# Performance work log

Measured on AMD Instinct MI355X. Metric: run time of the kernel, lower is better.

The kernel has to match this reference:

```python
import jax, jax.numpy as jnp
import numpy as np

FIELDS, NUM, CAT = 39, 13, 26
D, M, V, B, DEEP = 16, 16, 100000, 4096, 400
LEFT, RIGHT = np.triu_indices(FIELDS, k=1)  # pair indices, Q = 741
Q = LEFT.size
EPS = 1e-5


def setup_inputs() -> dict:
    key = jax.random.key(0)
    ks = jax.random.split(key, 18)
    xi = jax.random.randint(ks[0], (B, CAT), 0, V)
    xv = jax.random.uniform(ks[1], (B, NUM), dtype=jnp.float32)
    # 2nd-order embedding tables, stacked since all fields share vocab size
    emb_tables = jax.random.normal(ks[2], (FIELDS, V, D), dtype=jnp.float32) * 0.1
    T3 = jax.random.normal(ks[3], (D, M, D), dtype=jnp.float32) * 0.05
    T2 = jax.random.normal(ks[4], (M, D * D), dtype=jnp.float32) * 0.05
    gc = jax.random.normal(ks[5], (Q,), dtype=jnp.float32)
    fi_w = jax.random.normal(ks[6], (Q * M, DEEP), dtype=jnp.float32) * 0.01
    fi_b = jnp.zeros((DEEP,), dtype=jnp.float32)
    fi_gamma = jnp.ones((DEEP,), dtype=jnp.float32)
    fi_beta = jnp.zeros((DEEP,), dtype=jnp.float32)
    emb_w = jax.random.normal(ks[7], (FIELDS * D, DEEP), dtype=jnp.float32) * 0.02
    emb_b = jnp.zeros((DEEP,), dtype=jnp.float32)
    emb_gamma = jnp.ones((DEEP,), dtype=jnp.float32)
    emb_beta = jnp.zeros((DEEP,), dtype=jnp.float32)
    fc_w = jax.random.normal(ks[8], (2 * DEEP, 1), dtype=jnp.float32) * 0.05
    fc_b = jnp.zeros((1,), dtype=jnp.float32)
    return {"xi": xi, "xv": xv, "emb_tables": emb_tables, "T3": T3, "T2": T2,
            "gc": gc, "fi_w": fi_w, "fi_b": fi_b, "fi_gamma": fi_gamma, "fi_beta": fi_beta,
            "emb_w": emb_w, "emb_b": emb_b, "emb_gamma": emb_gamma, "emb_beta": emb_beta,
            "fc_w": fc_w, "fc_b": fc_b}


def _bn(x, gamma, beta):
    # BatchNorm1d in training mode: batch statistics, biased variance
    mean = jnp.mean(x, axis=0)
    var = jnp.var(x, axis=0)
    return gamma * (x - mean) * jax.lax.rsqrt(var + EPS) + beta


def reference(xi, xv, emb_tables, T3, T2, gc, fi_w, fi_b, fi_gamma, fi_beta,
              emb_w, emb_b, emb_gamma, emb_beta, fc_w, fc_b):
    # numerical fields: embedding row 0 scaled by the raw value
    num_part = xv[:, :, None] * emb_tables[:NUM, 0, :][None]          # [B, 13, D]
    # categorical fields: per-field gather
    cat_part = emb_tables[NUM + jnp.arange(CAT)[None, :], xi]          # [B, 26, D]
    fm2 = jnp.concatenate([num_part, cat_part], axis=1)               # [B, 39, D]
    vi = fm2[:, LEFT]                                                  # [B, Q, D]
    vj = fm2[:, RIGHT]                                                 # [B, Q, D]
    # einsum('bqd,dmd,bqd->bm'): repeated d on T3 takes its diagonal -> [D, M]
    T3diag = jnp.einsum('dmd->dm', T3)
    ga = jnp.einsum('bqd,bqd,dm->bm', vi, vj, T3diag)                  # [B, M]
    ga = jax.nn.softmax(ga, axis=1)
    # T1 = einsum('bm,mn->bmn'); s = einsum('bqd,bmn,bqd->bqm') sums T1 over n
    t1_rowsum = ga * jnp.sum(T2, axis=1)[None, :]                      # [B, M]
    pair_dot = jnp.einsum('bqd,bqd->bq', vi, vj)                       # [B, Q]
    s = pair_dot[:, :, None] * t1_rowsum[:, None, :]                   # [B, Q, M]
    sh = (s * gc[None, :, None]).reshape(-1, Q * M)                    # [B, Q*M]
    th = jax.nn.relu(_bn(sh @ fi_w + fi_b, fi_gamma, fi_beta))         # [B, DEEP]
    emb = fm2.reshape(-1, FIELDS * D)                                  # [B, 39*D]
    emb = jax.nn.relu(_bn(emb @ emb_w + emb_b, emb_gamma, emb_beta))   # [B, DEEP]
    out = jnp.concatenate([th, emb], axis=1) @ fc_w + fc_b             # [B, 1]
    return jnp.sum(jax.nn.sigmoid(out), axis=1)                        # [B]
```

## Files before the change

kernel.cpp:

```cpp
#include <hip/hip_runtime.h>
#include <hip/hip_bf16.h>

#define BATCH 4096
#define FIELDS_ 39
#define NUMF 13
#define CATF 26
#define DD 16
#define MM 16
#define VV 100000
#define DEEP_ 400
#define QQ 741
#define QPAD 768
#define KE 624
#define KEP 640
#define NEP 512
#define N1 6400
#define NKTE 20
#define NT_ 24
#define EPS_ 1e-5f

#define OFF_ABF 0
#define OFF_T   (BATCH*QPAD/2)
#define OFF_W2  (OFF_T + BATCH*MM)
#define OFF_WE  (OFF_W2 + N1*QPAD/2)
#define OFF_FMB (OFF_WE + NEP*KEP/2)
#define OFF_TH  (OFF_FMB + BATCH*KEP/2)
#define OFF_EMB (OFF_TH + BATCH*DEEP_)
#define OFF_ACC (OFF_EMB + BATCH*DEEP_)

typedef __attribute__((ext_vector_type(8))) short bf16x8;
typedef __attribute__((ext_vector_type(4))) float f32x4;

__device__ __forceinline__ ushort f2bf(float v) {
    union { float f; unsigned u; } x; x.f = v;
    unsigned r = x.u + 0x7fff + ((x.u >> 16) & 1);
    return (ushort)(r >> 16);
}
__device__ __forceinline__ unsigned pack2(float a, float b) {
    return (unsigned)f2bf(a) | ((unsigned)f2bf(b) << 16);
}
__device__ __forceinline__ void async16(void* lds, const void* g) {
    __builtin_amdgcn_global_load_lds(
        (const __attribute__((address_space(1))) unsigned int*)g,
        (__attribute__((address_space(3))) unsigned int*)lds,
        16, 0, 0);
}

__global__ __launch_bounds__(256) void kbig(const int* __restrict__ xi,
                                            const float* __restrict__ xv,
                                            const float* __restrict__ emb,
                                            const float* __restrict__ gc,
                                            const float* __restrict__ fi_w,
                                            const float* __restrict__ emb_w,
                                            const float* __restrict__ T3,
                                            const float* __restrict__ T2,
                                            float* __restrict__ ws,
                                            ushort* __restrict__ Abf,
                                            ushort* __restrict__ FMB,
                                            ushort* __restrict__ W2,
                                            ushort* __restrict__ WE) {
    __shared__ float smem[4200];
    int bid = blockIdx.x, tid = threadIdx.x;

    if (bid < BATCH) {
        float* row = smem;
        float* hsh = smem + 624;
        float* gash = smem + 640;
        ushort* stA = (ushort*)(smem + 656);
        ushort* stF = stA + QPAD;
        int b = bid;
        for (int e = tid; e < KE; e += 256) {
            int f = e >> 4, d = e & 15;
            float v;
            if (f < NUMF) {
                v = xv[b * NUMF + f] * emb[(long)f * VV * DD + d];
            } else {
                int c = f - NUMF;
                int idxv = xi[b * CATF + c];
                v = emb[((long)(NUMF + c) * VV + idxv) * DD + d];
            }
            row[e] = v;
        }
        __syncthreads();
        for (int e = tid; e < KEP; e += 256)
            stF[e] = (e < KE) ? f2bf(row[e]) : (ushort)0;
        if (tid < DD) {
            float s = 0.f, s2 = 0.f;
            for (int f = 0; f < FIELDS_; ++f) { float v = row[f * DD + tid]; s += v; s2 += v * v; }
            hsh[tid] = 0.5f * (s * s - s2);
        }
        __syncthreads();
        if (tid < MM) {
            float g = 0.f;
            for (int d = 0; d < DD; ++d) g += hsh[d] * T3[(d * MM + tid) * DD + d];
            gash[tid] = g;
        }
        __syncthreads();
        if (tid < MM) {
            float mx = -1e30f;
            for (int m = 0; m < MM; ++m) mx = fmaxf(mx, gash[m]);
            float se = 0.f;
            for (int m = 0; m < MM; ++m) se += expf(gash[m] - mx);
            ws[OFF_T + b * MM + tid] = expf(gash[tid] - mx) / se;
        }
        for (int q = tid; q < QPAD; q += 256) {
            float av = 0.f;
            if (q < QQ) {
                int i = 0, qq = q, cnt = FIELDS_ - 1;
                while (qq >= cnt) { qq -= cnt; ++i; cnt = FIELDS_ - 1 - i; }
                int j = i + 1 + qq;
                const float4* ri = (const float4*)&row[i * DD];
                const float4* rj = (const float4*)&row[j * DD];
                float4 a0 = ri[0], a1 = ri[1], a2 = ri[2], a3 = ri[3];
                float4 b0 = rj[0], b1 = rj[1], b2 = rj[2], b3 = rj[3];
                float dot = a0.x * b0.x + a0.y * b0.y + a0.z * b0.z + a0.w * b0.w
                          + a1.x * b1.x + a1.y * b1.y + a1.z * b1.z + a1.w * b1.w
                          + a2.x * b2.x + a2.y * b2.y + a2.z * b2.z + a2.w * b2.w
                          + a3.x * b3.x + a3.y * b3.y + a3.z * b3.z + a3.w * b3.w;
                av = dot * gc[q];
            }
            stA[q] = f2bf(av);
        }
        __syncthreads();
        if (tid < 96)
            *(uint4*)&Abf[(long)b * QPAD + tid * 8] = *(uint4*)&stA[tid * 8];
        else if (tid < 176)
            *(uint4*)&FMB[(long)b * KEP + (tid - 96) * 8] = *(uint4*)&stF[(tid - 96) * 8];
    } else if (bid < BATCH + 1536) {
        int bt = bid - BATCH;
        int kt = bt >> 6, m = (bt >> 2) & 15, ch = bt & 3;
        float* tile = smem;
        {
            float p = T2[m * DD * DD + tid];
#pragma unroll
            for (int off = 32; off > 0; off >>= 1) p += __shfl_down(p, off, 64);
            if ((tid & 63) == 0) smem[4100 + (tid >> 6)] = p;
        }
        for (int i = tid; i < 32 * 25; i += 256) {
            int ql = i / 25, c4 = i - ql * 25;
            int q = kt * 32 + ql;
            float4 v = make_float4(0.f, 0.f, 0.f, 0.f);
            if (q < QQ) v = *(const float4*)&fi_w[(q * MM + m) * DEEP_ + ch * 100 + c4 * 4];
            tile[ql * 101 + c4 * 4 + 0] = v.x; tile[ql * 101 + c4 * 4 + 1] = v.y;
            tile[ql * 101 + c4 * 4 + 2] = v.z; tile[ql * 101 + c4 * 4 + 3] = v.w;
        }
        __syncthreads();
        float t2s = smem[4100] + smem[4101] + smem[4102] + smem[4103];
        for (int i = tid; i < 100 * 4; i += 256) {
            int lc = i >> 2, cq = i & 3;
            int kcol = ch * 100 + lc;
            unsigned r[4];
#pragma unroll
            for (int j = 0; j < 4; ++j)
                r[j] = pack2(tile[(cq * 8 + 2 * j) * 101 + lc] * t2s,
                             tile[(cq * 8 + 2 * j + 1) * 101 + lc] * t2s);
            *(uint4*)&W2[(long)(kcol * 16 + m) * QPAD + kt * 32 + cq * 8] =
                make_uint4(r[0], r[1], r[2], r[3]);
        }
    } else {
        int bt = bid - BATCH - 1536;
        if (bt == 0) {
            for (int i = tid; i < 1600; i += 256) ws[OFF_ACC + i] = 0.f;
        }
        int kt = bt >> 2, ch = bt & 3;
        float* tile = smem;
        for (int i = tid; i < 32 * 32; i += 256) {
            int kl = i >> 5, c4 = i & 31;
            int k = kt * 32 + kl;
            int n = ch * 128 + c4 * 4;
            float4 v = make_float4(0.f, 0.f, 0.f, 0.f);
            if (k < KE && n < DEEP_) v = *(const float4*)&emb_w[k * DEEP_ + n];
            tile[kl * 129 + c4 * 4 + 0] = v.x; tile[kl * 129 + c4 * 4 + 1] = v.y;
            tile[kl * 129 + c4 * 4 + 2] = v.z; tile[kl * 129 + c4 * 4 + 3] = v.w;
        }
        __syncthreads();
        for (int i = tid; i < 128 * 4; i += 256) {
            int nl = i >> 2, cq = i & 3;
            int n = ch * 128 + nl;
            uint4 o = make_uint4(0, 0, 0, 0);
            if (n < DEEP_) {
                unsigned r[4];
#pragma unroll
                for (int j = 0; j < 4; ++j)
                    r[j] = pack2(tile[(cq * 8 + 2 * j) * 129 + nl], tile[(cq * 8 + 2 * j + 1) * 129 + nl]);
                o = make_uint4(r[0], r[1], r[2], r[3]);
            }
            if (n < NEP)
                *(uint4*)&WE[(long)n * KEP + kt * 32 + cq * 8] = o;
        }
    }
}

__device__ __forceinline__ void pipeline3(const ushort* p0, const ushort* p1,
                                          const ushort* p2, const ushort* p3,
                                          ushort* lds, int tid, int nt,
                                          int f1b, int f2b, int sw,
                                          f32x4 (*acc)[4]) {
#define STAGEP(SL, T) { \
    ushort* L_ = lds + (SL) * 16384; \
    async16(L_ + tid * 8,         p0 + (T) * 32); \
    async16(L_ + 4096 + tid * 8,  p1 + (T) * 32); \
    async16(L_ + 8192 + tid * 8,  p2 + (T) * 32); \
    async16(L_ + 12288 + tid * 8, p3 + (T) * 32); }
    STAGEP(0, 0); STAGEP(1, 1);
    asm volatile("s_waitcnt vmcnt(4)" ::: "memory");
    __builtin_amdgcn_s_barrier();
    int sl = 0;
    for (int t = 0; t < nt; ++t) {
        __builtin_amdgcn_sched_barrier(0);
        const ushort* cur = lds + sl * 16384;
        bf16x8 f1[8], f2[4];
#pragma unroll
        for (int r = 0; r < 8; ++r) f1[r] = *(const bf16x8*)&cur[f1b + r * 512 + sw];
#pragma unroll
        for (int c = 0; c < 4; ++c) f2[c] = *(const bf16x8*)&cur[f2b + c * 512 + sw];
        int sl2 = sl + 2; if (sl2 >= 3) sl2 -= 3;
        if (t + 2 < nt) STAGEP(sl2, t + 2);
        __builtin_amdgcn_s_setprio(1);
#pragma unroll
        for (int r = 0; r < 8; ++r)
#pragma unroll
            for (int c = 0; c < 4; ++c)
                acc[r][c] = __builtin_amdgcn_mfma_f32_16x16x32_bf16(f1[r], f2[c], acc[r][c], 0, 0, 0);
        __builtin_amdgcn_s_setprio(0);
        if (t + 1 < nt) {
            if (t + 2 < nt) { asm volatile("s_waitcnt vmcnt(4)" ::: "memory"); }
            else            { asm volatile("s_waitcnt vmcnt(0)" ::: "memory"); }
            __builtin_amdgcn_s_barrier();
        }
        sl = sl + 1; if (sl >= 3) sl -= 3;
    }
#undef STAGEP
}

__global__ __launch_bounds__(512, 2) void kgemms(const ushort* __restrict__ Abf,
                                                 const ushort* __restrict__ W2,
                                                 const ushort* __restrict__ FMB,
                                                 const ushort* __restrict__ WE,
                                                 const float* __restrict__ Tmat,
                                                 float* __restrict__ TH,
                                                 float* __restrict__ EMB,
                                                 float* __restrict__ ACC) {
    __shared__ ushort ldsbuf[3 * 16384];
    __shared__ float red[512];
    int tid = threadIdx.x;
    int lane = tid & 63, wid = tid >> 6;
    int wB = wid >> 2;
    int wS = wid & 3;
    int kq = lane >> 4, lr = lane & 15;
    int rr = tid >> 2, ac = tid & 3;
    int csw = (ac ^ ((rr >> 1) & 3)) * 8;
    int sw = (kq ^ ((lr >> 1) & 3)) * 8;
    red[tid] = 0.f;
    f32x4 acc[8][4] = {};
    int wg = blockIdx.x;

    if (wg < 400) {
        int s = (wg & 7) * 50 + (wg >> 3);
        int b0 = (s / 25) * 256;
        int n0 = (s % 25) * 256;
        const ushort* p0 = Abf + (long)(b0 + rr) * QPAD + csw;
        const ushort* p1 = Abf + (long)(b0 + 128 + rr) * QPAD + csw;
        const ushort* p2 = W2 + (long)(n0 + rr) * QPAD + csw;
        const ushort* p3 = W2 + (long)(n0 + 128 + rr) * QPAD + csw;
        pipeline3(p0, p1, p2, p3, ldsbuf, tid, NT_,
                  8192 + (wB * 128 + lr) * 32, (wS * 64 + lr) * 32, sw, acc);
        float* tbuf = (float*)ldsbuf;
        float ls[8] = {}, ls2[8] = {};
#pragma unroll
        for (int cg = 0; cg < 4; ++cg) {
            int bloc = wS * 64 + cg * 16 + lr;
            float4 t4 = *(const float4*)&Tmat[(b0 + bloc) * 16 + kq * 4];
#pragma unroll
            for (int r = 0; r < 8; ++r) {
                float v = acc[r][cg][0] * t4.x + acc[r][cg][1] * t4.y +
                          acc[r][cg][2] * t4.z + acc[r][cg][3] * t4.w;
                v += __shfl_xor(v, 16);
                v += __shfl_xor(v, 32);
                ls[r] += v; ls2[r] += v * v;
                if (lane < 16) tbuf[bloc * 17 + wB * 8 + r] = v;
            }
        }
#pragma unroll
        for (int r = 0; r < 8; ++r) {
            float a = ls[r], b2 = ls2[r];
            a += __shfl_xor(a, 8, 16); b2 += __shfl_xor(b2, 8, 16);
            a += __shfl_xor(a, 4, 16); b2 += __shfl_xor(b2, 4, 16);
            a += __shfl_xor(a, 2, 16); b2 += __shfl_xor(b2, 2, 16);
            a += __shfl_xor(a, 1, 16); b2 += __shfl_xor(b2, 1, 16);
            if (lane == 0) {
                atomicAdd(&red[wB * 8 + r], a);
                atomicAdd(&red[16 + wB * 8 + r], b2);
            }
        }
        __syncthreads();
        if (tid < 16) {
            atomicAdd(&ACC[(n0 >> 4) + tid], red[tid]);
            atomicAdd(&ACC[800 + (n0 >> 4) + tid], red[16 + tid]);
        }
        {
            int rowl = tid >> 1, kcb = (tid & 1) * 8;
            float o0 = tbuf[rowl * 17 + kcb + 0];
            float o1 = tbuf[rowl * 17 + kcb + 1];
            float o2 = tbuf[rowl * 17 + kcb + 2];
            float o3 = tbuf[rowl * 17 + kcb + 3];
            float o4 = tbuf[rowl * 17 + kcb + 4];
            float o5 = tbuf[rowl * 17 + kcb + 5];
            float o6 = tbuf[rowl * 17 + kcb + 6];
            float o7 = tbuf[rowl * 17 + kcb + 7];
            float* dst = &TH[(b0 + rowl) * DEEP_ + (n0 >> 4) + kcb];
            *(float4*)dst = make_float4(o0, o1, o2, o3);
            *(float4*)(dst + 4) = make_float4(o4, o5, o6, o7);
        }
    } else {
        int e = wg - 400;
        int se = (e & 7) * 4 + (e >> 3);
        int b0 = (se >> 1) * 256;
        int n0 = (se & 1) * 256;
        const ushort* p0 = FMB + (long)(b0 + rr) * KEP + csw;
        const ushort* p1 = FMB + (long)(b0 + 128 + rr) * KEP + csw;
        const ushort* p2 = WE + (long)(n0 + rr) * KEP + csw;
        const ushort* p3 = WE + (long)(n0 + 128 + rr) * KEP + csw;
        pipeline3(p0, p1, p2, p3, ldsbuf, tid, NKTE,
                  (wB * 128 + lr) * 32, 8192 + (wS * 64 + lr) * 32, sw, acc);
#pragma unroll
        for (int cg = 0; cg < 4; ++cg) {
            int ncl = wS * 64 + cg * 16 + lr;
            int nc = n0 + ncl;
            float ls = 0.f, ls2 = 0.f;
#pragma unroll
            for (int r = 0; r < 8; ++r) {
#pragma unroll
                for (int j = 0; j < 4; ++j) {
                    float v = acc[r][cg][j];
                    int brow = b0 + wB * 128 + r * 16 + kq * 4 + j;
                    if (nc < DEEP_) EMB[brow * DEEP_ + nc] = v;
                    ls += v; ls2 += v * v;
                }
            }
            ls += __shfl_xor(ls, 16);  ls += __shfl_xor(ls, 32);
            ls2 += __shfl_xor(ls2, 16); ls2 += __shfl_xor(ls2, 32);
            if (lane < 16 && nc < DEEP_) {
                atomicAdd(&red[ncl], ls);
                atomicAdd(&red[256 + ncl], ls2);
            }
        }
        __syncthreads();
        if (tid < 256) {
            int nc = n0 + tid;
            if (nc < DEEP_) {
                atomicAdd(&ACC[400 + nc], red[tid]);
                atomicAdd(&ACC[1200 + nc], red[256 + tid]);
            }
        }
    }
}

__global__ __launch_bounds__(256) void kfinal(const float* __restrict__ fig,
                                              const float* __restrict__ fibeta,
                                              const float* __restrict__ eg,
                                              const float* __restrict__ ebeta,
                                              const float* __restrict__ fcw,
                                              const float* __restrict__ fcb,
                                              const float* __restrict__ ws,
                                              float* __restrict__ out) {
    int b = blockIdx.x, tid = threadIdx.x;
    float part = 0.f;
    if (tid < 200) {
        int c = tid * 4;
        int loc = (c < DEEP_) ? c : c - DEEP_;
        const float* xp = (c < DEEP_) ? &ws[OFF_TH + b * DEEP_ + loc]
                                      : &ws[OFF_EMB + b * DEEP_ + loc];
        float4 x = *(const float4*)xp;
        float4 g = *(const float4*)((c < DEEP_) ? &fig[loc] : &eg[loc]);
        float4 be = *(const float4*)((c < DEEP_) ? &fibeta[loc] : &ebeta[loc]);
        float4 sm = *(const float4*)&ws[OFF_ACC + c];
        float4 sq = *(const float4*)&ws[OFF_ACC + 800 + c];
        float4 w = *(const float4*)&fcw[c];
        const float* xv_ = (const float*)&x; const float* gv = (const float*)&g;
        const float* bev = (const float*)&be; const float* smv = (const float*)&sm;
        const float* sqv = (const float*)&sq; const float* wv = (const float*)&w;
#pragma unroll
        for (int j = 0; j < 4; ++j) {
            float mean = smv[j] * (1.f / BATCH);
            float var = sqv[j] * (1.f / BATCH) - mean * mean;
            float rstd = rsqrtf(var + EPS_);
            float v = fmaxf(gv[j] * (xv_[j] - mean) * rstd + bev[j], 0.f);
            part += v * wv[j];
        }
    }
    __shared__ float red[4];
#pragma unroll
    for (int off = 32; off > 0; off >>= 1) part += __shfl_down(part, off, 64);
    if ((tid & 63) == 0) red[tid >> 6] = part;
    __syncthreads();
    if (tid == 0) {
        float tot = red[0] + red[1] + red[2] + red[3] + fcb[0];
        out[b] = 1.f / (1.f + expf(-tot));
    }
}

extern "C" void kernel_launch(void* const* d_in, const int* in_sizes, int n_in,
                              void* d_out, int out_size, void* d_ws, size_t ws_size,
                              hipStream_t stream) {
    const int*   xi    = (const int*)d_in[0];
    const float* xv    = (const float*)d_in[1];
    const float* emb   = (const float*)d_in[2];
    const float* T3    = (const float*)d_in[3];
    const float* T2    = (const float*)d_in[4];
    const float* gc    = (const float*)d_in[5];
    const float* fi_w  = (const float*)d_in[6];
    const float* fig   = (const float*)d_in[8];
    const float* fibt  = (const float*)d_in[9];
    const float* emb_w = (const float*)d_in[10];
    const float* eg    = (const float*)d_in[12];
    const float* ebt   = (const float*)d_in[13];
    const float* fcw   = (const float*)d_in[14];
    const float* fcb   = (const float*)d_in[15];
    float* ws = (float*)d_ws;
    ushort* Abf = (ushort*)(ws + OFF_ABF);
    ushort* W2  = (ushort*)(ws + OFF_W2);
    ushort* WE  = (ushort*)(ws + OFF_WE);
    ushort* FMB = (ushort*)(ws + OFF_FMB);
    float* out = (float*)d_out;

    hipLaunchKernelGGL(kbig, dim3(BATCH + 1536 + 80), dim3(256), 0, stream,
                       xi, xv, emb, gc, fi_w, emb_w, T3, T2, ws, Abf, FMB, W2, WE);
    hipLaunchKernelGGL(kgemms, dim3(432), dim3(512), 0, stream,
                       Abf, W2, FMB, WE, ws + OFF_T, ws + OFF_TH, ws + OFF_EMB, ws + OFF_ACC);
    hipLaunchKernelGGL(kfinal, dim3(BATCH), dim3(256), 0, stream,
                       fig, fibt, eg, ebt, fcw, fcb, ws, out);
}
```

Baseline: 83.74 us.

## Process one batch row per wavefront in feature and final kernels

Restructures the per-sample feature stage so each 64-lane wavefront handles one batch row, with four rows per block. Block-wide barriers and shared staging are replaced by wave shuffles for the pairwise-sum, gating and softmax reductions. The final BN/FC/sigmoid kernel is likewise mapped to one row per wavefront. This aims to cut block count, barrier stalls and idle threads, at the cost of narrower 2-byte global stores for the bf16 outputs.

After: 86.46 us. 3.3% more time.

```diff
diff --git a/kernel.cpp b/kernel.cpp
--- a/kernel.cpp
+++ b/kernel.cpp
@@ -62,14 +62,11 @@
     __shared__ float smem[4200];
     int bid = blockIdx.x, tid = threadIdx.x;
 
-    if (bid < BATCH) {
-        float* row = smem;
-        float* hsh = smem + 624;
-        float* gash = smem + 640;
-        ushort* stA = (ushort*)(smem + 656);
-        ushort* stF = stA + QPAD;
-        int b = bid;
-        for (int e = tid; e < KE; e += 256) {
+    if (bid < BATCH / 4) {
+        int wid = tid >> 6, lane = tid & 63;
+        int b = bid * 4 + wid;
+        float* row = smem + wid * 640;
+        for (int e = lane; e < KE; e += 64) {
             int f = e >> 4, d = e & 15;
             float v;
             if (f < NUMF) {
@@ -80,30 +77,40 @@
                 v = emb[((long)(NUMF + c) * VV + idxv) * DD + d];
             }
             row[e] = v;
-        }
-        __syncthreads();
-        for (int e = tid; e < KEP; e += 256)
-            stF[e] = (e < KE) ? f2bf(row[e]) : (ushort)0;
-        if (tid < DD) {
-            float s = 0.f, s2 = 0.f;
-            for (int f = 0; f < FIELDS_; ++f) { float v = row[f * DD + tid]; s += v; s2 += v * v; }
-            hsh[tid] = 0.5f * (s * s - s2);
-        }
-        __syncthreads();
-        if (tid < MM) {
-            float g = 0.f;
-            for (int d = 0; d < DD; ++d) g += hsh[d] * T3[(d * MM + tid) * DD + d];
-            gash[tid] = g;
-        }
-        __syncthreads();
-        if (tid < MM) {
-            float mx = -1e30f;
-            for (int m = 0; m < MM; ++m) mx = fmaxf(mx, gash[m]);
-            float se = 0.f;
-            for (int m = 0; m < MM; ++m) se += expf(gash[m] - mx);
-            ws[OFF_T + b * MM + tid] = expf(gash[tid] - mx) / se;
-        }
-        for (int q = tid; q < QPAD; q += 256) {
+            FMB[(long)b * KEP + e] = f2bf(v);
+        }
+        if (lane < KEP - KE) FMB[(long)b * KEP + KE + lane] = 0;
+        asm volatile("s_waitcnt lgkmcnt(0)" ::: "memory");
+        float s = 0.f, s2 = 0.f;
+        for (int e = lane; e < KE; e += 64) {
+            float v = row[e];
+            s += v; s2 += v * v;
+        }
+        s += __shfl_xor(s, 16);  s += __shfl_xor(s, 32);
+        s2 += __shfl_xor(s2, 16); s2 += __shfl_xor(s2, 32);
+        float h = 0.5f * (s * s - s2);
+        int r = lane & 15, g = lane >> 4;
+        float pg = 0.f;
+#pragma unroll
+        for (int j = 0; j < 4; ++j) {
+            int d = g + 4 * j;
+            float hd = __shfl(h, d, 16);
+            pg += hd * T3[(d * MM + r) * DD + d];
+        }
+        pg += __shfl_xor(pg, 16); pg += __shfl_xor(pg, 32);
+        float mx = pg;
+        mx = fmaxf(mx, __shfl_xor(mx, 1, 16));
+        mx = fmaxf(mx, __shfl_xor(mx, 2, 16));
+        mx = fmaxf(mx, __shfl_xor(mx, 4, 16));
+        mx = fmaxf(mx, __shfl_xor(mx, 8, 16));
+        float ex = expf(pg - mx);
+        float se = ex;
+        se += __shfl_xor(se, 1, 16);
+        se += __shfl_xor(se, 2, 16);
+        se += __shfl_xor(se, 4, 16);
+        se += __shfl_xor(se, 8, 16);
+        if (lane < 16) ws[OFF_T + b * MM + lane] = ex / se;
+        for (int q = lane; q < QPAD; q += 64) {
             float av = 0.f;
             if (q < QQ) {
                 int i = 0, qq = q, cnt = FIELDS_ - 1;
@@ -119,15 +126,10 @@
                           + a3.x * b3.x + a3.y * b3.y + a3.z * b3.z + a3.w * b3.w;
                 av = dot * gc[q];
             }
-            stA[q] = f2bf(av);
-        }
-        __syncthreads();
-        if (tid < 96)
-            *(uint4*)&Abf[(long)b * QPAD + tid * 8] = *(uint4*)&stA[tid * 8];
-        else if (tid < 176)
-            *(uint4*)&FMB[(long)b * KEP + (tid - 96) * 8] = *(uint4*)&stF[(tid - 96) * 8];
-    } else if (bid < BATCH + 1536) {
-        int bt = bid - BATCH;
+            Abf[(long)b * QPAD + q] = f2bf(av);
+        }
+    } else if (bid < BATCH / 4 + 1536) {
+        int bt = bid - BATCH / 4;
         int kt = bt >> 6, m = (bt >> 2) & 15, ch = bt & 3;
         float* tile = smem;
         {
@@ -158,7 +160,7 @@
                 make_uint4(r[0], r[1], r[2], r[3]);
         }
     } else {
-        int bt = bid - BATCH - 1536;
+        int bt = bid - BATCH / 4 - 1536;
         if (bt == 0) {
             for (int i = tid; i < 1600; i += 256) ws[OFF_ACC + i] = 0.f;
         }
@@ -364,10 +366,12 @@
                                               const float* __restrict__ fcb,
                                               const float* __restrict__ ws,
                                               float* __restrict__ out) {
-    int b = blockIdx.x, tid = threadIdx.x;
+    int tid = threadIdx.x;
+    int wid = tid >> 6, lane = tid & 63;
+    int b = blockIdx.x * 4 + wid;
     float part = 0.f;
-    if (tid < 200) {
-        int c = tid * 4;
+    for (int c4 = lane; c4 < 200; c4 += 64) {
+        int c = c4 * 4;
         int loc = (c < DEEP_) ? c : c - DEEP_;
         const float* xp = (c < DEEP_) ? &ws[OFF_TH + b * DEEP_ + loc]
                                       : &ws[OFF_EMB + b * DEEP_ + loc];
@@ -389,15 +393,9 @@
             part += v * wv[j];
         }
     }
-    __shared__ float red[4];
 #pragma unroll
     for (int off = 32; off > 0; off >>= 1) part += __shfl_down(part, off, 64);
-    if ((tid & 63) == 0) red[tid >> 6] = part;
-    __syncthreads();
-    if (tid == 0) {
-        float tot = red[0] + red[1] + red[2] + red[3] + fcb[0];
-        out[b] = 1.f / (1.f + expf(-tot));
-    }
+    if (lane == 0) out[b] = 1.f / (1.f + expf(-(part + fcb[0])));
 }
 
 extern "C" void kernel_launch(void* const* d_in, const int* in_sizes, int n_in,
@@ -424,10 +422,10 @@
     ushort* FMB = (ushort*)(ws + OFF_FMB);
     float* out = (float*)d_out;
 
-    hipLaunchKernelGGL(kbig, dim3(BATCH + 1536 + 80), dim3(256), 0, stream,
+    hipLaunchKernelGGL(kbig, dim3(BATCH / 4 + 1536 + 80), dim3(256), 0, stream,
                        xi, xv, emb, gc, fi_w, emb_w, T3, T2, ws, Abf, FMB, W2, WE);
     hipLaunchKernelGGL(kgemms, dim3(432), dim3(512), 0, stream,
                        Abf, W2, FMB, WE, ws + OFF_T, ws + OFF_TH, ws + OFF_EMB, ws + OFF_ACC);
-    hipLaunchKernelGGL(kfinal, dim3(BATCH), dim3(256), 0, stream,
+    hipLaunchKernelGGL(kfinal, dim3(BATCH / 4), dim3(256), 0, stream,
                        fig, fibt, eg, ebt, fcw, fcb, ws, out);
 }
```

## Restructure GEMM main loop into K=64 double-buffered tiles with interleaved phase staging

Applied to the files above, without the earlier changes.

Replaces the three-stage K=32 pipeline with a double-buffered K=64 scheme. Each tile is split into four MFMA phases, and the async global-to-LDS copies for the next tiles are interleaved across those phases with a new XOR swizzle. B fragments are held in registers across phases. LDS grows to 128KB and launch bounds drop to one block per CU, trading occupancy for fewer barriers per K and more overlap. The reduction scratch is moved into the reused LDS buffer after the loop.

Result: no change. 84.50 us (+0.9%).

```diff
diff --git a/kernel.cpp b/kernel.cpp
--- a/kernel.cpp
+++ b/kernel.cpp
@@ -15,8 +15,6 @@
 #define KEP 640
 #define NEP 512
 #define N1 6400
-#define NKTE 20
-#define NT_ 24
 #define EPS_ 1e-5f
 
 #define OFF_ABF 0
@@ -191,49 +189,7 @@
     }
 }
 
-__device__ __forceinline__ void pipeline3(const ushort* p0, const ushort* p1,
-                                          const ushort* p2, const ushort* p3,
-                                          ushort* lds, int tid, int nt,
-                                          int f1b, int f2b, int sw,
-                                          f32x4 (*acc)[4]) {
-#define STAGEP(SL, T) { \
-    ushort* L_ = lds + (SL) * 16384; \
-    async16(L_ + tid * 8,         p0 + (T) * 32); \
-    async16(L_ + 4096 + tid * 8,  p1 + (T) * 32); \
-    async16(L_ + 8192 + tid * 8,  p2 + (T) * 32); \
-    async16(L_ + 12288 + tid * 8, p3 + (T) * 32); }
-    STAGEP(0, 0); STAGEP(1, 1);
-    asm volatile("s_waitcnt vmcnt(4)" ::: "memory");
-    __builtin_amdgcn_s_barrier();
-    int sl = 0;
-    for (int t = 0; t < nt; ++t) {
-        __builtin_amdgcn_sched_barrier(0);
-        const ushort* cur = lds + sl * 16384;
-        bf16x8 f1[8], f2[4];
-#pragma unroll
-        for (int r = 0; r < 8; ++r) f1[r] = *(const bf16x8*)&cur[f1b + r * 512 + sw];
-#pragma unroll
-        for (int c = 0; c < 4; ++c) f2[c] = *(const bf16x8*)&cur[f2b + c * 512 + sw];
-        int sl2 = sl + 2; if (sl2 >= 3) sl2 -= 3;
-        if (t + 2 < nt) STAGEP(sl2, t + 2);
-        __builtin_amdgcn_s_setprio(1);
-#pragma unroll
-        for (int r = 0; r < 8; ++r)
-#pragma unroll
-            for (int c = 0; c < 4; ++c)
-                acc[r][c] = __builtin_amdgcn_mfma_f32_16x16x32_bf16(f1[r], f2[c], acc[r][c], 0, 0, 0);
-        __builtin_amdgcn_s_setprio(0);
-        if (t + 1 < nt) {
-            if (t + 2 < nt) { asm volatile("s_waitcnt vmcnt(4)" ::: "memory"); }
-            else            { asm volatile("s_waitcnt vmcnt(0)" ::: "memory"); }
-            __builtin_amdgcn_s_barrier();
-        }
-        sl = sl + 1; if (sl >= 3) sl -= 3;
-    }
-#undef STAGEP
-}
-
-__global__ __launch_bounds__(512, 2) void kgemms(const ushort* __restrict__ Abf,
+__global__ __launch_bounds__(512, 1) void kgemms(const ushort* __restrict__ Abf,
                                                  const ushort* __restrict__ W2,
                                                  const ushort* __restrict__ FMB,
                                                  const ushort* __restrict__ WE,
@@ -241,31 +197,106 @@
                                                  float* __restrict__ TH,
                                                  float* __restrict__ EMB,
                                                  float* __restrict__ ACC) {
-    __shared__ ushort ldsbuf[3 * 16384];
-    __shared__ float red[512];
+    __shared__ ushort ldsbuf[65536];
     int tid = threadIdx.x;
     int lane = tid & 63, wid = tid >> 6;
     int wB = wid >> 2;
     int wS = wid & 3;
     int kq = lane >> 4, lr = lane & 15;
-    int rr = tid >> 2, ac = tid & 3;
-    int csw = (ac ^ ((rr >> 1) & 3)) * 8;
-    int sw = (kq ^ ((lr >> 1) & 3)) * 8;
-    red[tid] = 0.f;
     f32x4 acc[8][4] = {};
     int wg = blockIdx.x;
 
-    if (wg < 400) {
+    long stride; const ushort *m0, *m1; int ntiles;
+    int b0, n0;
+    bool main_ = (wg < 400);
+    if (main_) {
         int s = (wg & 7) * 50 + (wg >> 3);
-        int b0 = (s / 25) * 256;
-        int n0 = (s % 25) * 256;
-        const ushort* p0 = Abf + (long)(b0 + rr) * QPAD + csw;
-        const ushort* p1 = Abf + (long)(b0 + 128 + rr) * QPAD + csw;
-        const ushort* p2 = W2 + (long)(n0 + rr) * QPAD + csw;
-        const ushort* p3 = W2 + (long)(n0 + 128 + rr) * QPAD + csw;
-        pipeline3(p0, p1, p2, p3, ldsbuf, tid, NT_,
-                  8192 + (wB * 128 + lr) * 32, (wS * 64 + lr) * 32, sw, acc);
+        b0 = (s / 25) * 256;
+        n0 = (s % 25) * 256;
+        m0 = Abf + (long)b0 * QPAD;
+        m1 = W2 + (long)n0 * QPAD;
+        stride = QPAD; ntiles = 12;
+    } else {
+        int e = wg - 400;
+        int se = (e & 7) * 4 + (e >> 3);
+        b0 = (se >> 1) * 256;
+        n0 = (se & 1) * 256;
+        m0 = WE + (long)n0 * KEP;
+        m1 = FMB + (long)b0 * KEP;
+        stride = KEP; ntiles = 10;
+    }
+
+    int cst = tid & 7, rl = tid >> 3;
+    int rowB_off = rl + ((rl & 32) ? 96 : 0);
+
+#define STAGE1(TILE, SEG) { \
+    int row_, mat_; \
+    if ((SEG) < 4) { mat_ = 0; row_ = (SEG) * 64 + rl; } \
+    else { mat_ = 1; row_ = ((SEG) - 4) * 32 + rowB_off; } \
+    int co_ = cst ^ (row_ & 7); \
+    const ushort* src_ = (mat_ ? m1 : m0) + (long)row_ * stride + (TILE) * 64 + co_ * 8; \
+    async16(&ldsbuf[((TILE) & 1) * 32768 + mat_ * 16384 + row_ * 64 + cst * 8], src_); }
+
+    int sz0 = ((kq) ^ (lr & 7)) * 8;
+    int sz1 = ((4 + kq) ^ (lr & 7)) * 8;
+    int a_off = (wS * 64 + lr) * 64;
+    int b_off = 16384 + (wB * 128 + lr) * 64;
+
+    bf16x8 f2r[4][2];
+
+#define PHASE(BUFI, R, DOF2, STG, VMC) { \
+    const ushort* bp_ = &ldsbuf[(BUFI) * 32768]; \
+    if (DOF2) { \
+        _Pragma("unroll") for (int c_ = 0; c_ < 4; ++c_) { \
+            f2r[c_][0] = *(const bf16x8*)&bp_[a_off + c_ * 1024 + sz0]; \
+            f2r[c_][1] = *(const bf16x8*)&bp_[a_off + c_ * 1024 + sz1]; } } \
+    bf16x8 f1_[2][2]; \
+    _Pragma("unroll") for (int j_ = 0; j_ < 2; ++j_) { \
+        f1_[j_][0] = *(const bf16x8*)&bp_[b_off + ((R) + j_) * 1024 + sz0]; \
+        f1_[j_][1] = *(const bf16x8*)&bp_[b_off + ((R) + j_) * 1024 + sz1]; } \
+    STG; \
+    __builtin_amdgcn_s_barrier(); \
+    asm volatile("s_waitcnt lgkmcnt(0)" ::: "memory"); \
+    __builtin_amdgcn_sched_barrier(0); \
+    __builtin_amdgcn_s_setprio(1); \
+    _Pragma("unroll") for (int j_ = 0; j_ < 2; ++j_) \
+    _Pragma("unroll") for (int c_ = 0; c_ < 4; ++c_) { \
+        acc[(R) + j_][c_] = __builtin_amdgcn_mfma_f32_16x16x32_bf16(f1_[j_][0], f2r[c_][0], acc[(R) + j_][c_], 0, 0, 0); \
+        acc[(R) + j_][c_] = __builtin_amdgcn_mfma_f32_16x16x32_bf16(f1_[j_][1], f2r[c_][1], acc[(R) + j_][c_], 0, 0, 0); } \
+    __builtin_amdgcn_s_setprio(0); \
+    VMC; \
+    __builtin_amdgcn_s_barrier(); }
+
+    for (int sg = 0; sg < 8; ++sg) STAGE1(0, sg);
+    for (int sg = 0; sg < 6; ++sg) STAGE1(1, sg);
+    asm volatile("s_waitcnt vmcnt(6)" ::: "memory");
+    __builtin_amdgcn_s_barrier();
+
+    int niter = ntiles >> 1;
+    for (int i = 0; i < niter; ++i) {
+        int t0 = 2 * i, t1 = 2 * i + 1;
+        bool more0 = (t0 + 2 < ntiles);
+        PHASE(0, 0, true,  { STAGE1(t1, 6); STAGE1(t1, 7); }, {});
+        PHASE(0, 2, false, { if (more0) { STAGE1(t0 + 2, 0); STAGE1(t0 + 2, 1); } }, {});
+        PHASE(0, 4, false, { if (more0) { STAGE1(t0 + 2, 2); STAGE1(t0 + 2, 3); } }, {});
+        PHASE(0, 6, false, { if (more0) { STAGE1(t0 + 2, 4); STAGE1(t0 + 2, 5); } },
+              { if (more0) { asm volatile("s_waitcnt vmcnt(6)" ::: "memory"); }
+                else       { asm volatile("s_waitcnt vmcnt(0)" ::: "memory"); } });
+        PHASE(1, 0, true,  { if (more0) { STAGE1(t0 + 2, 6); STAGE1(t0 + 2, 7); } }, {});
+        PHASE(1, 2, false, { if (more0) { STAGE1(t1 + 2, 0); STAGE1(t1 + 2, 1); } }, {});
+        PHASE(1, 4, false, { if (more0) { STAGE1(t1 + 2, 2); STAGE1(t1 + 2, 3); } }, {});
+        PHASE(1, 6, false, { if (more0) { STAGE1(t1 + 2, 4); STAGE1(t1 + 2, 5); } },
+              { if (more0) { asm volatile("s_waitcnt vmcnt(6)" ::: "memory"); } });
+    }
+#undef PHASE
+#undef STAGE1
+
+    __syncthreads();
+    float* red = (float*)&ldsbuf[32768];
+    if (main_) {
         float* tbuf = (float*)ldsbuf;
+        if (tid < 32) red[tid] = 0.f;
+        __syncthreads();
         float ls[8] = {}, ls2[8] = {};
 #pragma unroll
         for (int cg = 0; cg < 4; ++cg) {
@@ -313,16 +344,8 @@
             *(float4*)(dst + 4) = make_float4(o4, o5, o6, o7);
         }
     } else {
-        int e = wg - 400;
-        int se = (e & 7) * 4 + (e >> 3);
-        int b0 = (se >> 1) * 256;
-        int n0 = (se & 1) * 256;
-        const ushort* p0 = FMB + (long)(b0 + rr) * KEP + csw;
-        const ushort* p1 = FMB + (long)(b0 + 128 + rr) * KEP + csw;
-        const ushort* p2 = WE + (long)(n0 + rr) * KEP + csw;
-        const ushort* p3 = WE + (long)(n0 + 128 + rr) * KEP + csw;
-        pipeline3(p0, p1, p2, p3, ldsbuf, tid, NKTE,
-                  (wB * 128 + lr) * 32, 8192 + (wS * 64 + lr) * 32, sw, acc);
+        red[tid] = 0.f;
+        __syncthreads();
 #pragma unroll
         for (int cg = 0; cg < 4; ++cg) {
             int ncl = wS * 64 + cg * 16 + lr;
```
